# Kernel tuning notes

Measured on AMD Instinct MI355X. Metric: run time of the kernel, lower is better.

Reference implementation:

```python
import jax, jax.numpy as jnp
import numpy as np

HEADS = 4

def _unfold3x3(x):
    # x: [N, C, H, W] -> [N, C*9, H*W], channel-slowest / kernel-fastest (matches torch F.unfold)
    N, C, H, W = x.shape
    p = jnp.pad(x, ((0, 0), (0, 0), (1, 1), (1, 1)))
    pats = jnp.stack([p[:, :, i:i + H, j:j + W] for i in range(3) for j in range(3)], axis=2)
    return pats.reshape(N, C * 9, H * W)

def _conv1x1(x, w):
    # x: [N, Cin, H, W], w: [Cout, Cin]
    return jnp.einsum('nchw,oc->nohw', x, w)

def _dwconv3x3(x, w):
    # depthwise 3x3, x: [N, C, H, W], w: [C, 1, 3, 3]
    return jax.lax.conv_general_dilated(
        x, w, window_strides=(1, 1), padding='SAME',
        feature_group_count=x.shape[1],
        dimension_numbers=('NCHW', 'OIHW', 'NCHW'))

def _layernorm(x, w, b, eps=1e-5):
    m = jnp.mean(x, axis=-1, keepdims=True)
    v = jnp.mean(jnp.square(x - m), axis=-1, keepdims=True)
    return (x - m) * jax.lax.rsqrt(v + eps) * w + b

def _l2norm(x, eps=1e-12):
    n = jnp.sqrt(jnp.sum(jnp.square(x), axis=-1, keepdims=True))
    return x / jnp.maximum(n, eps)

def setup_inputs() -> dict:
    key = jax.random.key(0)
    ks = jax.random.split(key, 12)
    channels, angRes, h, w, b = 64, 5, 32, 32, 1
    a = angRes * angRes
    D = channels * 2          # 128
    hid = int(D * 2.66)       # 340
    s = 0.02
    return {
        'buffer': jax.random.normal(ks[0], (b, channels, a, h, w), jnp.float32),
        'mlp_w': jax.random.normal(ks[1], (D, channels * 9), jnp.float32) * s,
        'ln_attn_w': jnp.ones((D,), jnp.float32),
        'ln_attn_b': jnp.zeros((D,), jnp.float32),
        'ln_ffn_w': jnp.ones((D,), jnp.float32),
        'ln_ffn_b': jnp.zeros((D,), jnp.float32),
        'qkv_w': jax.random.normal(ks[2], (3 * D, D), jnp.float32) * s,
        'qkv_dw_w': jax.random.normal(ks[3], (3 * D, 1, 3, 3), jnp.float32) * s,
        'temperature': jnp.ones((HEADS, 1, 1), jnp.float32),
        'proj_attn_w': jax.random.normal(ks[4], (D, D), jnp.float32) * s,
        'ffn_in_w': jax.random.normal(ks[5], (2 * hid, D), jnp.float32) * s,
        'ffn_dw_w': jax.random.normal(ks[6], (2 * hid, 1, 3, 3), jnp.float32) * s,
        'ffn_out_w': jax.random.normal(ks[7], (D, hid), jnp.float32) * s,
        'proj3d_w': jax.random.normal(ks[8], (channels, D), jnp.float32) * s,
    }

def reference(buffer, mlp_w, ln_attn_w, ln_attn_b, ln_ffn_w, ln_ffn_b,
              qkv_w, qkv_dw_w, temperature, proj_attn_w,
              ffn_in_w, ffn_dw_w, ffn_out_w, proj3d_w):
    b, c, a, h, w = buffer.shape
    N, D = b * a, mlp_w.shape[0]
    L = h * w
    cph = D // HEADS

    # SAI2Token: [b,c,a,h,w] -> [(b a),c,h,w] -> unfold -> [L, N, c*9] -> MLP -> [L, N, D]
    buf2d = buffer.transpose(0, 2, 1, 3, 4).reshape(N, c, h, w)
    tok = _unfold3x3(buf2d).transpose(2, 0, 1)          # [L, N, c*9]
    tok = tok @ mlp_w.T                                  # [L, N, D]

    # --- attention branch ---
    tn = _layernorm(tok, ln_attn_w, ln_attn_b)
    x = tn.transpose(1, 2, 0).reshape(N, D, h, w)        # '(h w) n d -> n d h w'
    qkv = _dwconv3x3(_conv1x1(x, qkv_w), qkv_dw_w)       # [N, 3D, h, w]
    q, k, v = jnp.split(qkv, 3, axis=1)

    def heads(t):  # 'n (head c) h w -> n head (h w) c'
        return t.reshape(N, HEADS, cph, L).transpose(0, 1, 3, 2)
    q, k, v = heads(q), heads(k), heads(v)
    q, k = _l2norm(q), _l2norm(k)
    attn = jnp.einsum('nhlc,nhmc->nhlm', q, k) * temperature  # [N, HEADS, L, L]
    attn = jax.nn.softmax(attn, axis=-1)
    out = jnp.einsum('nhlm,nhmc->nhlc', attn, v)         # [N, HEADS, L, cph]
    out = out.transpose(0, 1, 3, 2).reshape(N, D, h, w)
    out = _conv1x1(out, proj_attn_w)
    tok = tok + out.reshape(N, D, L).transpose(2, 0, 1)

    # --- GDFN branch ---
    tf = _layernorm(tok, ln_ffn_w, ln_ffn_b)
    x2 = tf.transpose(1, 2, 0).reshape(N, D, h, w)
    y = _dwconv3x3(_conv1x1(x2, ffn_in_w), ffn_dw_w)     # [N, 2*hid, h, w]
    y1, y2 = jnp.split(y, 2, axis=1)
    y = jax.nn.gelu(y1, approximate=False) * y2
    y = _conv1x1(y, ffn_out_w)                           # [N, D, h, w]
    tok = tok + y.reshape(N, D, L).transpose(2, 0, 1)

    # Token2SAI: '(h w) (b a) d -> b d a h w' then 1x1x1 conv3d
    x5 = tok.reshape(h, w, b, a, D).transpose(2, 4, 3, 0, 1)  # [b, D, a, h, w]
    out = jnp.einsum('bdahw,od->boahw', x5, proj3d_w)
    return out
```

## Files before the change

### kernel.cpp

```cpp
#include <hip/hip_runtime.h>
#include <math.h>

#define M_TOK 25600

typedef __attribute__((ext_vector_type(8))) short bf16x8;
typedef __attribute__((ext_vector_type(4))) float f32x4;
typedef __attribute__((ext_vector_type(4))) int   i32x4;
typedef __attribute__((ext_vector_type(2))) int   i32x2;

__device__ __forceinline__ unsigned short f2b(float x) {
    unsigned u = __builtin_bit_cast(unsigned, x);
    return (unsigned short)((u + 0x7fffu + ((u >> 16) & 1u)) >> 16);
}
__device__ __forceinline__ float b2f(unsigned short h) {
    unsigned u = ((unsigned)h) << 16;
    return __builtin_bit_cast(float, u);
}
__device__ __forceinline__ unsigned cvtpk(float lo, float hi) {
    unsigned r;
    asm("v_cvt_pk_bf16_f32 %0, %1, %2" : "=v"(r) : "v"(lo), "v"(hi));
    return r;
}

__global__ __launch_bounds__(256) void prep_k(const float* __restrict__ s0, const float* __restrict__ s1,
                                              const float* __restrict__ s2, const float* __restrict__ s3,
                                              const float* __restrict__ s4, const float* __restrict__ s5,
                                              const float* __restrict__ qw, const float* __restrict__ fw,
                                              short* __restrict__ dst,
                                              float* __restrict__ wqT, float* __restrict__ wgT) {
    int i = blockIdx.x * 256 + threadIdx.x;
    if (i >= 297320) return;
    if (i < 287744) {
        if (i < 81920) {
            int r = i % 640, d = i / 640;
            int tap = r >> 6, cc = r & 63;
            dst[i] = (tap < 9) ? (short)f2b(s0[(d * 64 + cc) * 9 + tap]) : (short)0;
            return;
        }
        if (i >= 234496 && i < 279552) {
            int l = i - 234496;
            int row = l / 352, col = l % 352;
            dst[i] = (col < 340) ? (short)f2b(s4[row * 340 + col]) : (short)0;
            return;
        }
        const float* s; int off;
        if      (i < 131072) { s = s1; off = i - 81920; }
        else if (i < 147456) { s = s2; off = i - 131072; }
        else if (i < 234496) { s = s3; off = i - 147456; }
        else                 { s = s5; off = i - 279552; }
        dst[i] = (short)f2b(s[off]);
        return;
    }
    int j = i - 287744;
    if (j < 3456) {
        int tap = j / 384, c = j % 384;
        wqT[j] = qw[c * 9 + tap];
    } else {
        int k = j - 3456;
        int tap = k / 680, c = k % 680;
        wgT[k] = fw[c * 9 + tap];
    }
}

template <bool ADD, bool TROUT, bool AF32>
__global__ __launch_bounds__(256) void mm64_k(const void* __restrict__ Avp,
                                              const short* __restrict__ W,
                                              float* __restrict__ outp,
                                              int M, int N, int K) {
    __shared__ __align__(16) short As[2][64 * 40];
    __shared__ __align__(16) short Bs[2][64 * 40];
    const int tid = threadIdx.x;
    const int bm = blockIdx.x * 64;
    const int bn = blockIdx.y * 64;
    const int w = tid >> 6, lane = tid & 63;
    const int h = lane >> 4, l15 = lane & 15;
    const int wm = (w >> 1) * 32, wn = (w & 1) * 32;

    const int row = tid >> 2, c4 = tid & 3;
    const int gnW = bn + row;

    f32x4 acc[2][2];
#pragma unroll
    for (int i = 0; i < 2; ++i)
#pragma unroll
        for (int j = 0; j < 2; ++j) acc[i][j] = (f32x4){0.f, 0.f, 0.f, 0.f};

    short av[8], wv[8];

    auto ldA = [&](int k0, short* tmp) {
        int gk = k0 + c4 * 8;
        size_t abase = (size_t)(bm + row) * K + gk;
        if (AF32) {
            const float* ap = (const float*)Avp + abase;
            float4 va = *(const float4*)ap;
            float4 vb = *(const float4*)(ap + 4);
            tmp[0] = (short)f2b(va.x); tmp[1] = (short)f2b(va.y);
            tmp[2] = (short)f2b(va.z); tmp[3] = (short)f2b(va.w);
            tmp[4] = (short)f2b(vb.x); tmp[5] = (short)f2b(vb.y);
            tmp[6] = (short)f2b(vb.z); tmp[7] = (short)f2b(vb.w);
        } else {
            const short* ap = (const short*)Avp + abase;
            i32x2 a = *(const i32x2*)ap;
            i32x2 b = *(const i32x2*)(ap + 4);
            *(i32x2*)&tmp[0] = a; *(i32x2*)&tmp[4] = b;
        }
    };
    auto ldW = [&](int k0, short* tmp) {
        const short* wp = W + (size_t)gnW * K + k0 + c4 * 8;
        i32x2 a = *(const i32x2*)wp;
        i32x2 b = *(const i32x2*)(wp + 4);
        *(i32x2*)&tmp[0] = a; *(i32x2*)&tmp[4] = b;
    };

    ldA(0, av);
    ldW(0, wv);

    int ph = 0;
    for (int k0 = 0; k0 < K; k0 += 32, ph ^= 1) {
        *(i32x4*)&As[ph][row * 40 + c4 * 8] = *(i32x4*)av;
        *(i32x4*)&Bs[ph][row * 40 + c4 * 8] = *(i32x4*)wv;
        if (k0 + 32 < K) {
            ldA(k0 + 32, av);
            ldW(k0 + 32, wv);
        }
        __syncthreads();

        bf16x8 af[2], bf[2];
#pragma unroll
        for (int mi = 0; mi < 2; ++mi) af[mi] = *(const bf16x8*)&As[ph][(wm + mi * 16 + l15) * 40 + h * 8];
#pragma unroll
        for (int nj = 0; nj < 2; ++nj) bf[nj] = *(const bf16x8*)&Bs[ph][(wn + nj * 16 + l15) * 40 + h * 8];
#pragma unroll
        for (int mi = 0; mi < 2; ++mi)
#pragma unroll
            for (int nj = 0; nj < 2; ++nj) {
                if (TROUT)
                    acc[mi][nj] = __builtin_amdgcn_mfma_f32_16x16x32_bf16(bf[nj], af[mi], acc[mi][nj], 0, 0, 0);
                else
                    acc[mi][nj] = __builtin_amdgcn_mfma_f32_16x16x32_bf16(af[mi], bf[nj], acc[mi][nj], 0, 0, 0);
            }
    }

    if (!TROUT) {
#pragma unroll
        for (int mi = 0; mi < 2; ++mi) {
#pragma unroll
            for (int nj = 0; nj < 2; ++nj) {
                int gn = bn + wn + nj * 16 + l15;
#pragma unroll
                for (int r = 0; r < 4; ++r) {
                    int gm = bm + wm + mi * 16 + h * 4 + r;
                    size_t oi = (size_t)gm * N + gn;
                    if (ADD) outp[oi] += acc[mi][nj][r];
                    else     outp[oi] = acc[mi][nj][r];
                }
            }
        }
    } else {
#pragma unroll
        for (int mi = 0; mi < 2; ++mi) {
            int gm = bm + wm + mi * 16 + l15;
#pragma unroll
            for (int nj = 0; nj < 2; ++nj)
#pragma unroll
                for (int r = 0; r < 4; ++r) {
                    int gn = bn + wn + nj * 16 + h * 4 + r;
                    outp[(size_t)gn * M + gm] = acc[mi][nj][r];
                }
        }
    }
}

__global__ __launch_bounds__(256) void mmim_ln_k(const float* __restrict__ buf,
                                                 const short* __restrict__ W,
                                                 const float* __restrict__ lnw,
                                                 const float* __restrict__ lnb,
                                                 float* __restrict__ tok,
                                                 short* __restrict__ lnout) {
    const int K = 640;
    __shared__ __align__(16) short As[2][64 * 40];
    __shared__ __align__(16) short Bs[2][128 * 40];
    __shared__ float lnbuf[64][2][2];
    const int tid = threadIdx.x;
    const int bm = blockIdx.x * 64;
    const int w = tid >> 6, lane = tid & 63;
    const int h = lane >> 4, l15 = lane & 15;
    const int wr = w >> 1, wc = w & 1;
    const int wm = wr * 32, wn = wc * 64;

    const int rowA = tid >> 2, c4 = tid & 3;
    const int rowB1 = rowA + 64;

    f32x4 acc[2][4];
#pragma unroll
    for (int i = 0; i < 2; ++i)
#pragma unroll
        for (int j = 0; j < 4; ++j) acc[i][j] = (f32x4){0.f, 0.f, 0.f, 0.f};

    auto ldA = [&](int k0, short* tmp) {
        int t = bm + rowA;
        int l = t & 1023, n = t >> 10;
        int y = l >> 5, x = l & 31;
        int k = k0 + c4 * 8;
        int tap = k >> 6, cc0 = k & 63;
        bool ok = (tap < 9);
        int ti = 0, tj = 0;
        if (ok) { ti = tap / 3; tj = tap - ti * 3; }
        int yy = y + ti - 1, xx = x + tj - 1;
        ok = ok && (yy >= 0) && (yy < 32) && (xx >= 0) && (xx < 32);
        if (ok) {
            const float* bp = buf + (size_t)cc0 * M_TOK + (n << 10) + (yy << 5) + xx;
#pragma unroll
            for (int i = 0; i < 8; ++i) tmp[i] = (short)f2b(bp[(size_t)i * M_TOK]);
        } else {
#pragma unroll
            for (int i = 0; i < 8; ++i) tmp[i] = 0;
        }
    };
    auto ldW = [&](int row, int k0, short* tmp) {
        const short* wp = W + (size_t)row * K + k0 + c4 * 8;
        i32x2 a = *(const i32x2*)wp;
        i32x2 b = *(const i32x2*)(wp + 4);
        *(i32x2*)&tmp[0] = a; *(i32x2*)&tmp[4] = b;
    };
    auto compute = [&](int ph) {
        bf16x8 af[2], bf[4];
#pragma unroll
        for (int mi = 0; mi < 2; ++mi) af[mi] = *(const bf16x8*)&As[ph][(wm + mi * 16 + l15) * 40 + h * 8];
#pragma unroll
        for (int nj = 0; nj < 4; ++nj) bf[nj] = *(const bf16x8*)&Bs[ph][(wn + nj * 16 + l15) * 40 + h * 8];
#pragma unroll
        for (int mi = 0; mi < 2; ++mi)
#pragma unroll
            for (int nj = 0; nj < 4; ++nj)
                acc[mi][nj] = __builtin_amdgcn_mfma_f32_16x16x32_bf16(af[mi], bf[nj], acc[mi][nj], 0, 0, 0);
    };

    short aA[8], b0A[8], b1A[8];
    short aB[8], b0B[8], b1B[8];
    ldA(0, aA);  ldW(rowA, 0, b0A);  ldW(rowB1, 0, b1A);
    ldA(32, aB); ldW(rowA, 32, b0B); ldW(rowB1, 32, b1B);

    for (int k0 = 0; k0 < K; k0 += 64) {
        *(i32x4*)&As[0][rowA * 40 + c4 * 8]  = *(i32x4*)aA;
        *(i32x4*)&Bs[0][rowA * 40 + c4 * 8]  = *(i32x4*)b0A;
        *(i32x4*)&Bs[0][rowB1 * 40 + c4 * 8] = *(i32x4*)b1A;
        if (k0 + 64 < K) { ldA(k0 + 64, aA); ldW(rowA, k0 + 64, b0A); ldW(rowB1, k0 + 64, b1A); }
        __syncthreads();
        compute(0);
        *(i32x4*)&As[1][rowA * 40 + c4 * 8]  = *(i32x4*)aB;
        *(i32x4*)&Bs[1][rowA * 40 + c4 * 8]  = *(i32x4*)b0B;
        *(i32x4*)&Bs[1][rowB1 * 40 + c4 * 8] = *(i32x4*)b1B;
        if (k0 + 96 < K) { ldA(k0 + 96, aB); ldW(rowA, k0 + 96, b0B); ldW(rowB1, k0 + 96, b1B); }
        __syncthreads();
        compute(1);
    }

#pragma unroll
    for (int mi = 0; mi < 2; ++mi)
#pragma unroll
        for (int rr = 0; rr < 4; ++rr) {
            float s = 0.f, q = 0.f;
#pragma unroll
            for (int nj = 0; nj < 4; ++nj) {
                float v = acc[mi][nj][rr];
                s += v; q += v * v;
            }
#pragma unroll
            for (int off = 1; off < 16; off <<= 1) {
                s += __shfl_xor(s, off);
                q += __shfl_xor(q, off);
            }
            if (l15 == 0) {
                int rl = wm + mi * 16 + h * 4 + rr;
                lnbuf[rl][wc][0] = s;
                lnbuf[rl][wc][1] = q;
            }
        }
    __syncthreads();

    float wl[4], bl[4];
#pragma unroll
    for (int nj = 0; nj < 4; ++nj) {
        int gn = wn + nj * 16 + l15;
        wl[nj] = lnw[gn];
        bl[nj] = lnb[gn];
    }
#pragma unroll
    for (int mi = 0; mi < 2; ++mi)
#pragma unroll
        for (int rr = 0; rr < 4; ++rr) {
            int rl = wm + mi * 16 + h * 4 + rr;
            int gm = bm + rl;
            float S = lnbuf[rl][0][0] + lnbuf[rl][1][0];
            float Q = lnbuf[rl][0][1] + lnbuf[rl][1][1];
            float mean = S * (1.f / 128.f);
            float var = Q * (1.f / 128.f) - mean * mean;
            float rstd = rsqrtf(var + 1e-5f);
#pragma unroll
            for (int nj = 0; nj < 4; ++nj) {
                int gn = wn + nj * 16 + l15;
                float v = acc[mi][nj][rr];
                tok[(size_t)gm * 128 + gn] = v;
                float o = (v - mean) * rstd * wl[nj] + bl[nj];
                lnout[(size_t)gm * 128 + gn] = (short)f2b(o);
            }
        }
}

__global__ __launch_bounds__(256) void pmln_k(const short* __restrict__ A,
                                              const short* __restrict__ W,
                                              const float* __restrict__ lnw,
                                              const float* __restrict__ lnb,
                                              float* __restrict__ tok,
                                              short* __restrict__ lnout) {
    const int K = 128;
    __shared__ __align__(16) short As[2][64 * 40];
    __shared__ __align__(16) short Bs[2][128 * 40];
    __shared__ float lnbuf[64][2][2];
    const int tid = threadIdx.x;
    const int bm = blockIdx.x * 64;
    const int w = tid >> 6, lane = tid & 63;
    const int h = lane >> 4, l15 = lane & 15;
    const int wr = w >> 1, wc = w & 1;
    const int wm = wr * 32, wn = wc * 64;

    const int rowA = tid >> 2, c4 = tid & 3;
    const int rowB1 = rowA + 64;

    f32x4 acc[2][4];
#pragma unroll
    for (int i = 0; i < 2; ++i)
#pragma unroll
        for (int j = 0; j < 4; ++j) acc[i][j] = (f32x4){0.f, 0.f, 0.f, 0.f};

    auto ldA = [&](int k0, short* tmp) {
        const short* ap = A + (size_t)(bm + rowA) * K + k0 + c4 * 8;
        i32x2 a = *(const i32x2*)ap;
        i32x2 b = *(const i32x2*)(ap + 4);
        *(i32x2*)&tmp[0] = a; *(i32x2*)&tmp[4] = b;
    };
    auto ldW = [&](int row, int k0, short* tmp) {
        const short* wp = W + (size_t)row * K + k0 + c4 * 8;
        i32x2 a = *(const i32x2*)wp;
        i32x2 b = *(const i32x2*)(wp + 4);
        *(i32x2*)&tmp[0] = a; *(i32x2*)&tmp[4] = b;
    };
    auto compute = [&](int ph) {
        bf16x8 af[2], bf[4];
#pragma unroll
        for (int mi = 0; mi < 2; ++mi) af[mi] = *(const bf16x8*)&As[ph][(wm + mi * 16 + l15) * 40 + h * 8];
#pragma unroll
        for (int nj = 0; nj < 4; ++nj) bf[nj] = *(const bf16x8*)&Bs[ph][(wn + nj * 16 + l15) * 40 + h * 8];
#pragma unroll
        for (int mi = 0; mi < 2; ++mi)
#pragma unroll
            for (int nj = 0; nj < 4; ++nj)
                acc[mi][nj] = __builtin_amdgcn_mfma_f32_16x16x32_bf16(af[mi], bf[nj], acc[mi][nj], 0, 0, 0);
    };

    short aA[8], b0A[8], b1A[8];
    short aB[8], b0B[8], b1B[8];
    ldA(0, aA);  ldW(rowA, 0, b0A);  ldW(rowB1, 0, b1A);
    ldA(32, aB); ldW(rowA, 32, b0B); ldW(rowB1, 32, b1B);

    for (int k0 = 0; k0 < K; k0 += 64) {
        *(i32x4*)&As[0][rowA * 40 + c4 * 8]  = *(i32x4*)aA;
        *(i32x4*)&Bs[0][rowA * 40 + c4 * 8]  = *(i32x4*)b0A;
        *(i32x4*)&Bs[0][rowB1 * 40 + c4 * 8] = *(i32x4*)b1A;
        if (k0 + 64 < K) { ldA(k0 + 64, aA); ldW(rowA, k0 + 64, b0A); ldW(rowB1, k0 + 64, b1A); }
        __syncthreads();
        compute(0);
        *(i32x4*)&As[1][rowA * 40 + c4 * 8]  = *(i32x4*)aB;
        *(i32x4*)&Bs[1][rowA * 40 + c4 * 8]  = *(i32x4*)b0B;
        *(i32x4*)&Bs[1][rowB1 * 40 + c4 * 8] = *(i32x4*)b1B;
        if (k0 + 96 < K) { ldA(k0 + 96, aB); ldW(rowA, k0 + 96, b0B); ldW(rowB1, k0 + 96, b1B); }
        __syncthreads();
        compute(1);
    }

#pragma unroll
    for (int mi = 0; mi < 2; ++mi)
#pragma unroll
        for (int rr = 0; rr < 4; ++rr) {
            int gm = bm + wm + mi * 16 + h * 4 + rr;
#pragma unroll
            for (int nj = 0; nj < 4; ++nj) {
                int gn = wn + nj * 16 + l15;
                acc[mi][nj][rr] += tok[(size_t)gm * 128 + gn];
            }
        }
#pragma unroll
    for (int mi = 0; mi < 2; ++mi)
#pragma unroll
        for (int rr = 0; rr < 4; ++rr) {
            float s = 0.f, q = 0.f;
#pragma unroll
            for (int nj = 0; nj < 4; ++nj) {
                float v = acc[mi][nj][rr];
                s += v; q += v * v;
            }
#pragma unroll
            for (int off = 1; off < 16; off <<= 1) {
                s += __shfl_xor(s, off);
                q += __shfl_xor(q, off);
            }
            if (l15 == 0) {
                int rl = wm + mi * 16 + h * 4 + rr;
                lnbuf[rl][wc][0] = s;
                lnbuf[rl][wc][1] = q;
            }
        }
    __syncthreads();

    float wl[4], bl[4];
#pragma unroll
    for (int nj = 0; nj < 4; ++nj) {
        int gn = wn + nj * 16 + l15;
        wl[nj] = lnw[gn];
        bl[nj] = lnb[gn];
    }
#pragma unroll
    for (int mi = 0; mi < 2; ++mi)
#pragma unroll
        for (int rr = 0; rr < 4; ++rr) {
            int rl = wm + mi * 16 + h * 4 + rr;
            int gm = bm + rl;
            float S = lnbuf[rl][0][0] + lnbuf[rl][1][0];
            float Q = lnbuf[rl][0][1] + lnbuf[rl][1][1];
            float mean = S * (1.f / 128.f);
            float var = Q * (1.f / 128.f) - mean * mean;
            float rstd = rsqrtf(var + 1e-5f);
#pragma unroll
            for (int nj = 0; nj < 4; ++nj) {
                int gn = wn + nj * 16 + l15;
                float v = acc[mi][nj][rr];
                tok[(size_t)gm * 128 + gn] = v;
                float o = (v - mean) * rstd * wl[nj] + bl[nj];
                lnout[(size_t)gm * 128 + gn] = (short)f2b(o);
            }
        }
}

__global__ __launch_bounds__(256) void mmw_k(const short* __restrict__ A,
                                             const short* __restrict__ W,
                                             short* __restrict__ outp,
                                             int M, int N, int K) {
    __shared__ __align__(16) short As[2][128 * 40];
    __shared__ __align__(16) short Bs[2][128 * 40];
    const int tid = threadIdx.x;
    const int bm = blockIdx.x * 128;
    const int bn = blockIdx.y * 128;
    const int w = tid >> 6, lane = tid & 63;
    const int h = lane >> 4, l15 = lane & 15;
    const int wm = (w >> 1) * 64, wn = (w & 1) * 64;

    const int row0 = tid >> 2, c4 = tid & 3;
    const int row1 = row0 + 64;

    f32x4 acc[4][4];
#pragma unroll
    for (int i = 0; i < 4; ++i)
#pragma unroll
        for (int j = 0; j < 4; ++j) acc[i][j] = (f32x4){0.f, 0.f, 0.f, 0.f};

    auto ldA = [&](int row, int k0, short* tmp) {
        const short* ap = A + (size_t)(bm + row) * K + k0 + c4 * 8;
        i32x2 x = *(const i32x2*)ap;
        i32x2 y = *(const i32x2*)(ap + 4);
        *(i32x2*)&tmp[0] = x; *(i32x2*)&tmp[4] = y;
    };
    auto ldW = [&](int row, int k0, short* tmp) {
        int gn = bn + row;
        if (gn < N) {
            const short* wp = W + (size_t)gn * K + k0 + c4 * 8;
            i32x2 x = *(const i32x2*)wp;
            i32x2 y = *(const i32x2*)(wp + 4);
            *(i32x2*)&tmp[0] = x; *(i32x2*)&tmp[4] = y;
        } else {
#pragma unroll
            for (int i = 0; i < 8; ++i) tmp[i] = 0;
        }
    };
    auto compute = [&](int ph) {
        bf16x8 af[4], bf[4];
#pragma unroll
        for (int mi = 0; mi < 4; ++mi) af[mi] = *(const bf16x8*)&As[ph][(wm + mi * 16 + l15) * 40 + h * 8];
#pragma unroll
        for (int nj = 0; nj < 4; ++nj) bf[nj] = *(const bf16x8*)&Bs[ph][(wn + nj * 16 + l15) * 40 + h * 8];
#pragma unroll
        for (int mi = 0; mi < 4; ++mi)
#pragma unroll
            for (int nj = 0; nj < 4; ++nj)
                acc[mi][nj] = __builtin_amdgcn_mfma_f32_16x16x32_bf16(af[mi], bf[nj], acc[mi][nj], 0, 0, 0);
    };

    short a0A[8], a1A[8], b0A[8], b1A[8];
    short a0B[8], a1B[8], b0B[8], b1B[8];
    ldA(row0, 0, a0A);  ldA(row1, 0, a1A);  ldW(row0, 0, b0A);  ldW(row1, 0, b1A);
    ldA(row0, 32, a0B); ldA(row1, 32, a1B); ldW(row0, 32, b0B); ldW(row1, 32, b1B);

    for (int k0 = 0; k0 < K; k0 += 64) {
        *(i32x4*)&As[0][row0 * 40 + c4 * 8] = *(i32x4*)a0A;
        *(i32x4*)&As[0][row1 * 40 + c4 * 8] = *(i32x4*)a1A;
        *(i32x4*)&Bs[0][row0 * 40 + c4 * 8] = *(i32x4*)b0A;
        *(i32x4*)&Bs[0][row1 * 40 + c4 * 8] = *(i32x4*)b1A;
        if (k0 + 64 < K) {
            ldA(row0, k0 + 64, a0A); ldA(row1, k0 + 64, a1A);
            ldW(row0, k0 + 64, b0A); ldW(row1, k0 + 64, b1A);
        }
        __syncthreads();
        compute(0);
        *(i32x4*)&As[1][row0 * 40 + c4 * 8] = *(i32x4*)a0B;
        *(i32x4*)&As[1][row1 * 40 + c4 * 8] = *(i32x4*)a1B;
        *(i32x4*)&Bs[1][row0 * 40 + c4 * 8] = *(i32x4*)b0B;
        *(i32x4*)&Bs[1][row1 * 40 + c4 * 8] = *(i32x4*)b1B;
        if (k0 + 96 < K) {
            ldA(row0, k0 + 96, a0B); ldA(row1, k0 + 96, a1B);
            ldW(row0, k0 + 96, b0B); ldW(row1, k0 + 96, b1B);
        }
        __syncthreads();
        compute(1);
    }

#pragma unroll
    for (int mi = 0; mi < 4; ++mi) {
#pragma unroll
        for (int nj = 0; nj < 4; ++nj) {
            int gn = bn + wn + nj * 16 + l15;
            if (gn < N) {
#pragma unroll
                for (int r = 0; r < 4; ++r) {
                    int gm = bm + wm + mi * 16 + h * 4 + r;
                    outp[(size_t)gm * N + gn] = (short)f2b(acc[mi][nj][r]);
                }
            }
        }
    }
}

__global__ __launch_bounds__(256) void dwl2n_k(const short* __restrict__ in,
                                               const float* __restrict__ wqT,
                                               const float* __restrict__ temp,
                                               short* __restrict__ out) {
    int idx = blockIdx.x * 256 + threadIdx.x;
    int q = idx % 48;
    int t = idx / 48;
    int c0 = q * 8;
    int l = t & 1023, n = t >> 10;
    int y = l >> 5, x = l & 31;
    int tb = n << 10;

    float acc[8];
#pragma unroll
    for (int k = 0; k < 8; ++k) acc[k] = 0.f;

#pragma unroll
    for (int i = 0; i < 3; ++i) {
        int yy = y + i - 1;
        if (yy < 0 || yy >= 32) continue;
#pragma unroll
        for (int j = 0; j < 3; ++j) {
            int xx = x + j - 1;
            if (xx < 0 || xx >= 32) continue;
            bf16x8 d = *(const bf16x8*)(in + (size_t)(tb + (yy << 5) + xx) * 384 + c0);
            float4 wa = *(const float4*)(wqT + (i * 3 + j) * 384 + c0);
            float4 wb = *(const float4*)(wqT + (i * 3 + j) * 384 + c0 + 4);
            acc[0] += b2f((unsigned short)d[0]) * wa.x;
            acc[1] += b2f((unsigned short)d[1]) * wa.y;
            acc[2] += b2f((unsigned short)d[2]) * wa.z;
            acc[3] += b2f((unsigned short)d[3]) * wa.w;
            acc[4] += b2f((unsigned short)d[4]) * wb.x;
            acc[5] += b2f((unsigned short)d[5]) * wb.y;
            acc[6] += b2f((unsigned short)d[6]) * wb.z;
            acc[7] += b2f((unsigned short)d[7]) * wb.w;
        }
    }
    float ss = 0.f;
#pragma unroll
    for (int k = 0; k < 8; ++k) ss += acc[k] * acc[k];
    ss += __shfl_xor(ss, 1);
    ss += __shfl_xor(ss, 2);
    float sc;
    if (c0 < 128)       sc = (1.f / fmaxf(sqrtf(ss), 1e-12f)) * temp[c0 >> 5] * 1.44269504089f;
    else if (c0 < 256)  sc = 1.f / fmaxf(sqrtf(ss), 1e-12f);
    else                sc = 1.f;
    unsigned o[4];
#pragma unroll
    for (int k = 0; k < 4; ++k)
        o[k] = f2b(acc[2 * k] * sc) | ((unsigned)f2b(acc[2 * k + 1] * sc) << 16);
    *(i32x4*)(out + (size_t)t * 384 + c0) = *(i32x4*)o;
}

__global__ __launch_bounds__(256) void gdfn2_k(const short* __restrict__ in,
                                               const float* __restrict__ wgT,
                                               short* __restrict__ out) {
    int idx = blockIdx.x * 256 + threadIdx.x;
    int q = idx % 44;
    int t = idx / 44;
    int c0 = q * 8;
    short* op = out + (size_t)t * 352 + c0;
    if (q == 43) {
        *(i32x4*)op = (i32x4){0, 0, 0, 0};
        return;
    }
    int l = t & 1023, n = t >> 10;
    int y = l >> 5, x = l & 31;
    int tb = n << 10;

    float a[8], g[8];
#pragma unroll
    for (int k = 0; k < 8; ++k) { a[k] = 0.f; g[k] = 0.f; }

#pragma unroll
    for (int i = 0; i < 3; ++i) {
        int yy = y + i - 1;
        if (yy < 0 || yy >= 32) continue;
#pragma unroll
        for (int j = 0; j < 3; ++j) {
            int xx = x + j - 1;
            if (xx < 0 || xx >= 32) continue;
            const short* p = in + (size_t)(tb + (yy << 5) + xx) * 680 + c0;
            bf16x8 d1 = *(const bf16x8*)p;
            i32x2 d2a = *(const i32x2*)(p + 340);
            i32x2 d2b = *(const i32x2*)(p + 344);
            short d2[8];
            *(i32x2*)&d2[0] = d2a; *(i32x2*)&d2[4] = d2b;
            const float* wp = wgT + (i * 3 + j) * 680 + c0;
            float4 w1a = *(const float4*)wp;
            float4 w1b = *(const float4*)(wp + 4);
            float w1[8] = {w1a.x, w1a.y, w1a.z, w1a.w, w1b.x, w1b.y, w1b.z, w1b.w};
            float w2[8];
#pragma unroll
            for (int k = 0; k < 8; ++k) w2[k] = wp[340 + k];
#pragma unroll
            for (int k = 0; k < 8; ++k) {
                a[k] += b2f((unsigned short)d1[k]) * w1[k];
                g[k] += b2f((unsigned short)d2[k]) * w2[k];
            }
        }
    }
    unsigned o[4];
#pragma unroll
    for (int k = 0; k < 4; ++k) {
        float r0 = 0.5f * a[2 * k] * (1.f + erff(a[2 * k] * 0.70710678118f)) * g[2 * k];
        float r1 = 0.5f * a[2 * k + 1] * (1.f + erff(a[2 * k + 1] * 0.70710678118f)) * g[2 * k + 1];
        o[k] = f2b(r0) | ((unsigned)f2b(r1) << 16);
    }
    if (q == 42) { o[2] = 0; o[3] = 0; }
    *(i32x4*)op = *(i32x4*)o;
}

__global__ __launch_bounds__(256) void attn_k(const short* __restrict__ qkv,
                                              short* __restrict__ outp) {
    __shared__ __align__(16) short Ks[2][64 * 40];
    __shared__ __align__(16) short Vp[2][2048];
    const int b = blockIdx.x;
    const int orig = (b & 7) * 200 + (b >> 3);
    const int qt = orig & 15, nh = orig >> 4;
    const int hd = nh & 3, n = nh >> 2;
    const int tid = threadIdx.x;
    const int w = tid >> 6, lane = tid & 63;
    const int h = lane >> 4, l15 = lane & 15;
    const size_t base = (size_t)n * 1024 * 384;
    const int qrow = qt * 64 + w * 16 + l15;

    bf16x8 qf = *(const bf16x8*)(qkv + base + (size_t)qrow * 384 + hd * 32 + h * 8);
    f32x4 o0 = {0.f,0.f,0.f,0.f}, o1 = {0.f,0.f,0.f,0.f};
    f32x4 osum = {0.f,0.f,0.f,0.f};
    union { unsigned u[4]; bf16x8 v; } ones;
#pragma unroll
    for (int r = 0; r < 4; ++r) ones.u[r] = 0x3F803F80u;

    const int skey = tid >> 2, sc4 = tid & 3;
    const int sg = skey >> 5, skey5 = skey & 31;
    const int sh = (skey5 >> 2) & 3;
    const int sj = (skey5 & 3) + ((skey5 >> 4) << 2);
    const int sgran0 = (sg * 4 + sh) * 32 + sc4 * 8;
    const short* kbase = qkv + base + (size_t)skey * 384 + 128 + hd * 32 + sc4 * 8;

    auto scatterV = [&](int nb, i32x4 vreg) {
        short vs[8];
        *(i32x4*)vs = vreg;
#pragma unroll
        for (int i = 0; i < 8; ++i) {
            int gran = sgran0 + i;
            gran ^= (gran >> 3) & 7;
            Vp[nb][gran * 8 + sj] = vs[i];
        }
    };
    auto compute = [&](int nb) {
        const bf16x8 kf0 = *(const bf16x8*)&Ks[nb][l15 * 40 + h * 8];
        const bf16x8 kf1 = *(const bf16x8*)&Ks[nb][(16 + l15) * 40 + h * 8];
        const bf16x8 kf2 = *(const bf16x8*)&Ks[nb][(32 + l15) * 40 + h * 8];
        const bf16x8 kf3 = *(const bf16x8*)&Ks[nb][(48 + l15) * 40 + h * 8];
        int gr0 = h * 32 + l15;            gr0 ^= (gr0 >> 3) & 7;
        int gr1 = h * 32 + 16 + l15;       gr1 ^= (gr1 >> 3) & 7;
        int gr2 = (4 + h) * 32 + l15;      gr2 ^= (gr2 >> 3) & 7;
        int gr3 = (4 + h) * 32 + 16 + l15; gr3 ^= (gr3 >> 3) & 7;
        const bf16x8 va0 = *(const bf16x8*)&Vp[nb][gr0 * 8];
        const bf16x8 va1 = *(const bf16x8*)&Vp[nb][gr1 * 8];
        const bf16x8 vb0 = *(const bf16x8*)&Vp[nb][gr2 * 8];
        const bf16x8 vb1 = *(const bf16x8*)&Vp[nb][gr3 * 8];
        const f32x4 z = {0.f, 0.f, 0.f, 0.f};

        __builtin_amdgcn_s_setprio(1);
        f32x4 s0 = __builtin_amdgcn_mfma_f32_16x16x32_bf16(kf0, qf, z, 0, 0, 0);
        f32x4 s1 = __builtin_amdgcn_mfma_f32_16x16x32_bf16(kf1, qf, z, 0, 0, 0);
        f32x4 s2 = __builtin_amdgcn_mfma_f32_16x16x32_bf16(kf2, qf, z, 0, 0, 0);
        f32x4 s3 = __builtin_amdgcn_mfma_f32_16x16x32_bf16(kf3, qf, z, 0, 0, 0);
        __builtin_amdgcn_s_setprio(0);
        float p[16];
#pragma unroll
        for (int r = 0; r < 4; ++r) {
            p[r]      = exp2f(s0[r]);
            p[4 + r]  = exp2f(s1[r]);
            p[8 + r]  = exp2f(s2[r]);
            p[12 + r] = exp2f(s3[r]);
        }
        union { unsigned u[4]; bf16x8 v; } pf1, pf2;
#pragma unroll
        for (int r = 0; r < 4; ++r) {
            pf1.u[r] = cvtpk(p[2 * r], p[2 * r + 1]);
            pf2.u[r] = cvtpk(p[8 + 2 * r], p[8 + 2 * r + 1]);
        }
        __builtin_amdgcn_s_setprio(1);
        osum = __builtin_amdgcn_mfma_f32_16x16x32_bf16(ones.v, pf1.v, osum, 0, 0, 0);
        osum = __builtin_amdgcn_mfma_f32_16x16x32_bf16(ones.v, pf2.v, osum, 0, 0, 0);
        o0 = __builtin_amdgcn_mfma_f32_16x16x32_bf16(va0, pf1.v, o0, 0, 0, 0);
        o1 = __builtin_amdgcn_mfma_f32_16x16x32_bf16(va1, pf1.v, o1, 0, 0, 0);
        o0 = __builtin_amdgcn_mfma_f32_16x16x32_bf16(vb0, pf2.v, o0, 0, 0, 0);
        o1 = __builtin_amdgcn_mfma_f32_16x16x32_bf16(vb1, pf2.v, o1, 0, 0, 0);
        __builtin_amdgcn_s_setprio(0);
    };

    i32x4 kregA = *(const i32x4*)kbase;
    i32x4 vregA = *(const i32x4*)(kbase + 128);
    i32x4 kregB = *(const i32x4*)(kbase + (size_t)64 * 384);
    i32x4 vregB = *(const i32x4*)(kbase + (size_t)64 * 384 + 128);

    for (int t = 0; t < 16; t += 2) {
        *(i32x4*)&Ks[0][skey * 40 + sc4 * 8] = kregA;
        scatterV(0, vregA);
        if (t + 2 < 16) {
            const short* kp = kbase + (size_t)(t + 2) * 64 * 384;
            kregA = *(const i32x4*)kp;
            vregA = *(const i32x4*)(kp + 128);
        }
        __syncthreads();
        compute(0);
        *(i32x4*)&Ks[1][skey * 40 + sc4 * 8] = kregB;
        scatterV(1, vregB);
        if (t + 3 < 16) {
            const short* kp = kbase + (size_t)(t + 3) * 64 * 384;
            kregB = *(const i32x4*)kp;
            vregB = *(const i32x4*)(kp + 128);
        }
        __syncthreads();
        compute(1);
    }

    float inv = 1.f / osum[0];

    size_t ob = ((size_t)n * 1024 + qrow) * 128 + hd * 32;
    unsigned u;
    u = f2b(o0[0] * inv) | ((unsigned)f2b(o0[1] * inv) << 16); *(unsigned*)(outp + ob + h * 4) = u;
    u = f2b(o0[2] * inv) | ((unsigned)f2b(o0[3] * inv) << 16); *(unsigned*)(outp + ob + h * 4 + 2) = u;
    u = f2b(o1[0] * inv) | ((unsigned)f2b(o1[1] * inv) << 16); *(unsigned*)(outp + ob + 16 + h * 4) = u;
    u = f2b(o1[2] * inv) | ((unsigned)f2b(o1[3] * inv) << 16); *(unsigned*)(outp + ob + 16 + h * 4 + 2) = u;
}

extern "C" void kernel_launch(void* const* d_in, const int* in_sizes, int n_in,
                              void* d_out, int out_size, void* d_ws, size_t ws_size,
                              hipStream_t stream) {
    const float* buffer      = (const float*)d_in[0];
    const float* mlp_w       = (const float*)d_in[1];
    const float* ln_attn_w   = (const float*)d_in[2];
    const float* ln_attn_b   = (const float*)d_in[3];
    const float* ln_ffn_w    = (const float*)d_in[4];
    const float* ln_ffn_b    = (const float*)d_in[5];
    const float* qkv_w       = (const float*)d_in[6];
    const float* qkv_dw_w    = (const float*)d_in[7];
    const float* temperature = (const float*)d_in[8];
    const float* proj_attn_w = (const float*)d_in[9];
    const float* ffn_in_w    = (const float*)d_in[10];
    const float* ffn_dw_w    = (const float*)d_in[11];
    const float* ffn_out_w   = (const float*)d_in[12];
    const float* proj3d_w    = (const float*)d_in[13];

    char* wsb = (char*)d_ws;
    short* Wbf     = (short*)wsb;
    short* mlpW    = Wbf;
    short* qkvW    = Wbf + 81920;
    short* projW   = Wbf + 131072;
    short* ffnInW  = Wbf + 147456;
    short* ffnOutW = Wbf + 234496;
    short* p3dW    = Wbf + 279552;
    float* wqT     = (float*)(wsb + 575488);
    float* wgT     = (float*)(wsb + 589312);
    float* tok     = (float*)(wsb + 33381792);
    short* LNbf    = (short*)(wsb + 46488992);
    short* QKVpre  = (short*)(wsb + 53042592);
    short* qkvb    = (short*)(wsb + 72703392);
    short* AObf    = (short*)(wsb + 92364192);
    short* F1      = (short*)(wsb + 98917792);
    short* G       = (short*)(wsb + 133733792);

    dim3 blk(256);

    prep_k<<<1162, blk, 0, stream>>>(mlp_w, qkv_w, proj_attn_w, ffn_in_w, ffn_out_w, proj3d_w,
                                     qkv_dw_w, ffn_dw_w, Wbf, wqT, wgT);

    mmim_ln_k<<<400, blk, 0, stream>>>(buffer, mlpW, ln_attn_w, ln_attn_b, tok, LNbf);
    mmw_k<<<dim3(200, 3), blk, 0, stream>>>(LNbf, qkvW, QKVpre, M_TOK, 384, 128);
    dwl2n_k<<<4800, blk, 0, stream>>>(QKVpre, wqT, temperature, qkvb);
    attn_k<<<1600, blk, 0, stream>>>(qkvb, AObf);
    pmln_k<<<400, blk, 0, stream>>>(AObf, projW, ln_ffn_w, ln_ffn_b, tok, LNbf);
    mmw_k<<<dim3(200, 6), blk, 0, stream>>>(LNbf, ffnInW, F1, M_TOK, 680, 128);
    gdfn2_k<<<4400, blk, 0, stream>>>(F1, wgT, G);
    mm64_k<true, false, false><<<dim3(400, 2), blk, 0, stream>>>(G, ffnOutW, tok, M_TOK, 128, 352);
    mm64_k<false, true, true><<<dim3(400, 1), blk, 0, stream>>>(tok, p3dW, (float*)d_out, M_TOK, 64, 128);
}
```

Baseline: 183.5 us.

## Fuse FFN output GEMM, residual add, and proj3d GEMM into one kernel

The FFN out-projection, residual add into tok, and the final proj3d projection now run in one kernel instead of two mm64 launches. Each block computes a 64-row tile of the full 128-wide FFN output, adds the residual, keeps the result as bf16 in shared memory, then multiplies by the proj3d weights and writes the transposed output. This drops the fp32 read-modify-write of tok, the re-read of tok, and one launch. In exchange tok is no longer updated in global memory, and the shared-memory footprint per block grows.

```diff
diff --git a/kernel.cpp b/kernel.cpp
--- a/kernel.cpp
+++ b/kernel.cpp
@@ -59,115 +59,6 @@
         int k = j - 3456;
         int tap = k / 680, c = k % 680;
         wgT[k] = fw[c * 9 + tap];
-    }
-}
-
-template <bool ADD, bool TROUT, bool AF32>
-__global__ __launch_bounds__(256) void mm64_k(const void* __restrict__ Avp,
-                                              const short* __restrict__ W,
-                                              float* __restrict__ outp,
-                                              int M, int N, int K) {
-    __shared__ __align__(16) short As[2][64 * 40];
-    __shared__ __align__(16) short Bs[2][64 * 40];
-    const int tid = threadIdx.x;
-    const int bm = blockIdx.x * 64;
-    const int bn = blockIdx.y * 64;
-    const int w = tid >> 6, lane = tid & 63;
-    const int h = lane >> 4, l15 = lane & 15;
-    const int wm = (w >> 1) * 32, wn = (w & 1) * 32;
-
-    const int row = tid >> 2, c4 = tid & 3;
-    const int gnW = bn + row;
-
-    f32x4 acc[2][2];
-#pragma unroll
-    for (int i = 0; i < 2; ++i)
-#pragma unroll
-        for (int j = 0; j < 2; ++j) acc[i][j] = (f32x4){0.f, 0.f, 0.f, 0.f};
-
-    short av[8], wv[8];
-
-    auto ldA = [&](int k0, short* tmp) {
-        int gk = k0 + c4 * 8;
-        size_t abase = (size_t)(bm + row) * K + gk;
-        if (AF32) {
-            const float* ap = (const float*)Avp + abase;
-            float4 va = *(const float4*)ap;
-            float4 vb = *(const float4*)(ap + 4);
-            tmp[0] = (short)f2b(va.x); tmp[1] = (short)f2b(va.y);
-            tmp[2] = (short)f2b(va.z); tmp[3] = (short)f2b(va.w);
-            tmp[4] = (short)f2b(vb.x); tmp[5] = (short)f2b(vb.y);
-            tmp[6] = (short)f2b(vb.z); tmp[7] = (short)f2b(vb.w);
-        } else {
-            const short* ap = (const short*)Avp + abase;
-            i32x2 a = *(const i32x2*)ap;
-            i32x2 b = *(const i32x2*)(ap + 4);
-            *(i32x2*)&tmp[0] = a; *(i32x2*)&tmp[4] = b;
-        }
-    };
-    auto ldW = [&](int k0, short* tmp) {
-        const short* wp = W + (size_t)gnW * K + k0 + c4 * 8;
-        i32x2 a = *(const i32x2*)wp;
-        i32x2 b = *(const i32x2*)(wp + 4);
-        *(i32x2*)&tmp[0] = a; *(i32x2*)&tmp[4] = b;
-    };
-
-    ldA(0, av);
-    ldW(0, wv);
-
-    int ph = 0;
-    for (int k0 = 0; k0 < K; k0 += 32, ph ^= 1) {
-        *(i32x4*)&As[ph][row * 40 + c4 * 8] = *(i32x4*)av;
-        *(i32x4*)&Bs[ph][row * 40 + c4 * 8] = *(i32x4*)wv;
-        if (k0 + 32 < K) {
-            ldA(k0 + 32, av);
-            ldW(k0 + 32, wv);
-        }
-        __syncthreads();
-
-        bf16x8 af[2], bf[2];
-#pragma unroll
-        for (int mi = 0; mi < 2; ++mi) af[mi] = *(const bf16x8*)&As[ph][(wm + mi * 16 + l15) * 40 + h * 8];
-#pragma unroll
-        for (int nj = 0; nj < 2; ++nj) bf[nj] = *(const bf16x8*)&Bs[ph][(wn + nj * 16 + l15) * 40 + h * 8];
-#pragma unroll
-        for (int mi = 0; mi < 2; ++mi)
-#pragma unroll
-            for (int nj = 0; nj < 2; ++nj) {
-                if (TROUT)
-                    acc[mi][nj] = __builtin_amdgcn_mfma_f32_16x16x32_bf16(bf[nj], af[mi], acc[mi][nj], 0, 0, 0);
-                else
-                    acc[mi][nj] = __builtin_amdgcn_mfma_f32_16x16x32_bf16(af[mi], bf[nj], acc[mi][nj], 0, 0, 0);
-            }
-    }
-
-    if (!TROUT) {
-#pragma unroll
-        for (int mi = 0; mi < 2; ++mi) {
-#pragma unroll
-            for (int nj = 0; nj < 2; ++nj) {
-                int gn = bn + wn + nj * 16 + l15;
-#pragma unroll
-                for (int r = 0; r < 4; ++r) {
-                    int gm = bm + wm + mi * 16 + h * 4 + r;
-                    size_t oi = (size_t)gm * N + gn;
-                    if (ADD) outp[oi] += acc[mi][nj][r];
-                    else     outp[oi] = acc[mi][nj][r];
-                }
-            }
-        }
-    } else {
-#pragma unroll
-        for (int mi = 0; mi < 2; ++mi) {
-            int gm = bm + wm + mi * 16 + l15;
-#pragma unroll
-            for (int nj = 0; nj < 2; ++nj)
-#pragma unroll
-                for (int r = 0; r < 4; ++r) {
-                    int gn = bn + wn + nj * 16 + h * 4 + r;
-                    outp[(size_t)gn * M + gm] = acc[mi][nj][r];
-                }
-        }
     }
 }
 
@@ -440,6 +331,127 @@
                 lnout[(size_t)gm * 128 + gn] = (short)f2b(o);
             }
         }
+}
+
+__global__ __launch_bounds__(256) void fmt2s_k(const short* __restrict__ G,
+                                               const short* __restrict__ Wf,
+                                               const short* __restrict__ Wp,
+                                               const float* __restrict__ tok,
+                                               float* __restrict__ outp) {
+    const int K = 352;
+    __shared__ __align__(16) short As[2][64 * 40];
+    __shared__ __align__(16) short Bs[2][128 * 40];
+    __shared__ __align__(16) short Tbf[64][136];
+    const int tid = threadIdx.x;
+    const int bm = blockIdx.x * 64;
+    const int w = tid >> 6, lane = tid & 63;
+    const int h = lane >> 4, l15 = lane & 15;
+    const int wr = w >> 1, wc = w & 1;
+    const int wm = wr * 32, wn = wc * 64;
+
+    const int rowA = tid >> 2, c4 = tid & 3;
+    const int rowB1 = rowA + 64;
+
+    f32x4 acc[2][4];
+#pragma unroll
+    for (int i = 0; i < 2; ++i)
+#pragma unroll
+        for (int j = 0; j < 4; ++j) acc[i][j] = (f32x4){0.f, 0.f, 0.f, 0.f};
+
+    short av[8], b0[8], b1[8];
+
+    auto ldA = [&](int k0, short* tmp) {
+        const short* ap = G + (size_t)(bm + rowA) * K + k0 + c4 * 8;
+        i32x2 a = *(const i32x2*)ap;
+        i32x2 b = *(const i32x2*)(ap + 4);
+        *(i32x2*)&tmp[0] = a; *(i32x2*)&tmp[4] = b;
+    };
+    auto ldW = [&](int row, int k0, short* tmp) {
+        const short* wp = Wf + (size_t)row * K + k0 + c4 * 8;
+        i32x2 a = *(const i32x2*)wp;
+        i32x2 b = *(const i32x2*)(wp + 4);
+        *(i32x2*)&tmp[0] = a; *(i32x2*)&tmp[4] = b;
+    };
+
+    ldA(0, av);
+    ldW(rowA, 0, b0);
+    ldW(rowB1, 0, b1);
+
+    int ph = 0;
+    for (int k0 = 0; k0 < K; k0 += 32, ph ^= 1) {
+        *(i32x4*)&As[ph][rowA * 40 + c4 * 8]  = *(i32x4*)av;
+        *(i32x4*)&Bs[ph][rowA * 40 + c4 * 8]  = *(i32x4*)b0;
+        *(i32x4*)&Bs[ph][rowB1 * 40 + c4 * 8] = *(i32x4*)b1;
+        if (k0 + 32 < K) {
+            ldA(k0 + 32, av);
+            ldW(rowA, k0 + 32, b0);
+            ldW(rowB1, k0 + 32, b1);
+        }
+        __syncthreads();
+
+        bf16x8 af[2], bf[4];
+#pragma unroll
+        for (int mi = 0; mi < 2; ++mi) af[mi] = *(const bf16x8*)&As[ph][(wm + mi * 16 + l15) * 40 + h * 8];
+#pragma unroll
+        for (int nj = 0; nj < 4; ++nj) bf[nj] = *(const bf16x8*)&Bs[ph][(wn + nj * 16 + l15) * 40 + h * 8];
+#pragma unroll
+        for (int mi = 0; mi < 2; ++mi)
+#pragma unroll
+            for (int nj = 0; nj < 4; ++nj)
+                acc[mi][nj] = __builtin_amdgcn_mfma_f32_16x16x32_bf16(af[mi], bf[nj], acc[mi][nj], 0, 0, 0);
+    }
+
+    __syncthreads();
+#pragma unroll
+    for (int mi = 0; mi < 2; ++mi)
+#pragma unroll
+        for (int rr = 0; rr < 4; ++rr) {
+            int rl = wm + mi * 16 + h * 4 + rr;
+            int gm = bm + rl;
+#pragma unroll
+            for (int nj = 0; nj < 4; ++nj) {
+                int gn = wn + nj * 16 + l15;
+                float v = acc[mi][nj][rr] + tok[(size_t)gm * 128 + gn];
+                Tbf[rl][gn] = (short)f2b(v);
+            }
+        }
+    __syncthreads();
+
+    f32x4 acc2[2][2];
+#pragma unroll
+    for (int i = 0; i < 2; ++i)
+#pragma unroll
+        for (int j = 0; j < 2; ++j) acc2[i][j] = (f32x4){0.f, 0.f, 0.f, 0.f};
+
+#pragma unroll
+    for (int ks = 0; ks < 4; ++ks) {
+        bf16x8 af2[2], bf2[2];
+#pragma unroll
+        for (int mi = 0; mi < 2; ++mi)
+            af2[mi] = *(const bf16x8*)&Tbf[wm + mi * 16 + l15][ks * 32 + h * 8];
+#pragma unroll
+        for (int nj = 0; nj < 2; ++nj) {
+            int o = wc * 32 + nj * 16 + l15;
+            bf2[nj] = *(const bf16x8*)(Wp + (size_t)o * 128 + ks * 32 + h * 8);
+        }
+#pragma unroll
+        for (int mi = 0; mi < 2; ++mi)
+#pragma unroll
+            for (int nj = 0; nj < 2; ++nj)
+                acc2[mi][nj] = __builtin_amdgcn_mfma_f32_16x16x32_bf16(bf2[nj], af2[mi], acc2[mi][nj], 0, 0, 0);
+    }
+
+#pragma unroll
+    for (int mi = 0; mi < 2; ++mi) {
+        int gt = bm + wm + mi * 16 + l15;
+#pragma unroll
+        for (int nj = 0; nj < 2; ++nj)
+#pragma unroll
+            for (int r = 0; r < 4; ++r) {
+                int o = wc * 32 + nj * 16 + h * 4 + r;
+                outp[(size_t)o * M_TOK + gt] = acc2[mi][nj][r];
+            }
+    }
 }
 
 __global__ __launch_bounds__(256) void mmw_k(const short* __restrict__ A,
@@ -818,6 +830,5 @@
     pmln_k<<<400, blk, 0, stream>>>(AObf, projW, ln_ffn_w, ln_ffn_b, tok, LNbf);
     mmw_k<<<dim3(200, 6), blk, 0, stream>>>(LNbf, ffnInW, F1, M_TOK, 680, 128);
     gdfn2_k<<<4400, blk, 0, stream>>>(F1, wgT, G);
-    mm64_k<true, false, false><<<dim3(400, 2), blk, 0, stream>>>(G, ffnOutW, tok, M_TOK, 128, 352);
-    mm64_k<false, true, true><<<dim3(400, 1), blk, 0, stream>>>(tok, p3dW, (float*)d_out, M_TOK, 64, 128);
-}
+    fmt2s_k<<<400, blk, 0, stream>>>(G, ffnOutW, p3dW, tok, (float*)d_out);
+}
```

Measured after the change: 176.5 us (median of 2 runs). -3.8%, faster.
